# Kernel optimization log

Measured on AMD Instinct MI355X. Metric: run time of the kernel, lower is better.

## Reference

```python
import jax, jax.numpy as jnp
import numpy as np

B, L, H, V, HALF = 128, 4096, 64, 64, 32
ALPHA = 0.95
LN_EPS = 1e-5


def _normalize(x):
    # torch F.normalize(dim=-1): x / max(||x||_2, 1e-12)
    n = jnp.linalg.norm(x, axis=-1, keepdims=True)
    return x / jnp.maximum(n, 1e-12)


def setup_inputs() -> dict:
    key = jax.random.key(0)
    ks = jax.random.split(key, 17)
    s = 0.05
    return {
        "seq": jax.random.randint(ks[0], (B, L), 0, V),
        "embed": jax.random.normal(ks[1], (V, H), jnp.float32),
        "W1": jax.random.normal(ks[2], (H, 2 * H), jnp.float32) * s,
        "b1": jnp.zeros((2 * H,), jnp.float32),
        "W2": jax.random.normal(ks[3], (2 * H, H), jnp.float32) * s,
        "b2": jnp.zeros((H,), jnp.float32),
        "gamma": jnp.ones((H,), jnp.float32),
        "beta": jnp.zeros((H,), jnp.float32),
        "Ws": jax.random.normal(ks[4], (H, HALF), jnp.float32) * s,
        "bs": jnp.zeros((HALF,), jnp.float32),
        "We": jax.random.normal(ks[5], (H, HALF), jnp.float32) * s,
        "be": jnp.zeros((HALF,), jnp.float32),
        "Wrp": jax.random.normal(ks[6], (2 * HALF, H), jnp.float32) * s,
        "brp": jnp.zeros((H,), jnp.float32),
        "Wout": jax.random.normal(ks[7], (H, V), jnp.float32) * s,
        "bout": jnp.zeros((V,), jnp.float32),
    }


def _forward(seq, embed, W1, b1, W2, b2, gamma, beta,
             Ws, bs, We, be, Wrp, brp, Wout, bout):
    # Encoder: embed + FF(ReLU) residual + LayerNorm
    h0 = embed[seq]                                   # [B,L,H]
    ff = jnp.maximum(h0 @ W1 + b1, 0.0) @ W2 + b2
    x = h0 + ff
    mu = x.mean(-1, keepdims=True)
    var = ((x - mu) ** 2).mean(-1, keepdims=True)
    h = (x - mu) / jnp.sqrt(var + LN_EPS) * gamma + beta  # [B,L,H]

    # Precompute per-step projections for t = 0 .. L-2
    hp = h[:, :-1, :]                                 # [B,L-1,H]
    hs = hp @ Ws + bs                                 # [B,L-1,HALF]
    he = hp @ We + be
    ksn = _normalize(hs)
    ken = _normalize(he)
    scale = (jnp.arange(L - 1, dtype=h.dtype) + 1.0) / L  # (t+1)/L

    def step(carry, inp):
        M_s, M_e = carry                              # [B,HALF,HALF]
        hs_t, he_t, ks_t, ke_t, sc = inp
        vps = jnp.einsum('bij,bj->bi', M_s, ks_t)
        vpe = jnp.einsum('bij,bj->bi', M_e, ke_t)
        M_s = M_s + (1.0 - ALPHA) * (hs_t - vps)[:, :, None] * ks_t[:, None, :]
        M_e = M_e + (1.0 - ALPHA) * sc * (he_t - vpe)[:, :, None] * ke_t[:, None, :]
        return (M_s, M_e), None

    xs = (jnp.swapaxes(hs, 0, 1), jnp.swapaxes(he, 0, 1),
          jnp.swapaxes(ksn, 0, 1), jnp.swapaxes(ken, 0, 1), scale)
    M0 = jnp.zeros((B, HALF, HALF), h.dtype)
    (M_s, M_e), _ = jax.lax.scan(step, (M0, M0), xs)

    # Read with last-token query
    q = h[:, -1, :]
    qs = _normalize(q @ Ws + bs)
    qe = _normalize(q @ We + be)
    rs = jnp.einsum('bij,bj->bi', M_s, qs)
    re = jnp.einsum('bij,bj->bi', M_e, qe)
    r = jnp.concatenate([rs, re], axis=-1)            # [B,2*HALF]
    return (r @ Wrp + brp) @ Wout + bout              # [B,V]


def reference(seq, embed, W1, b1, W2, b2, gamma, beta,
              Ws, bs, We, be, Wrp, brp, Wout, bout):
    return _forward(seq, embed, W1, b1, W2, b2, gamma, beta,
                    Ws, bs, We, be, Wrp, brp, Wout, bout)
```

## Files before the change

### kernel.cpp

```cpp
#include <hip/hip_runtime.h>
#include <hip/hip_bf16.h>
#include <stdint.h>


#define BETA 0.05f
#define NB 128
#define NL 4096
#define TC 16
#define NCH 256
#define NBLD 6
#define SLOT_F 1360
#define NSLOT 12

#define L_GR   (NSLOT * SLOT_F)
#define L_DA   (L_GR + 4096)
#define L_RV   (L_DA + 64)
#define L_O1   (L_RV + 64)
#define L_WHO  (L_O1 + 64)
#define L_TOT  (L_WHO + 1)

struct Ptrs { const void* p[15]; };

__device__ inline float readlane_f(float v, int l) {
    return __int_as_float(__builtin_amdgcn_readlane(__float_as_int(v), l));
}
__device__ inline float bperm_f(int idx, float v) {
    return __int_as_float(__builtin_amdgcn_ds_bpermute(idx, __float_as_int(v)));
}
__device__ inline float ldT(const float* p, int i) { return p[i]; }
__device__ inline float ldT(const __hip_bfloat16* p, int i) { return __bfloat162float(p[i]); }

template <typename T>
__device__ void build_tables_body(const T* emb, const T* W1, const T* b1,
                                  const T* W2, const T* b2, const T* gam,
                                  const T* bet, const T* Wsm, const T* bsv,
                                  const T* Wem, const T* bev, float* tbl)
{
    int v = blockIdx.x;
    int j = threadIdx.x;
    __shared__ float h0s[64];
    __shared__ float act[128];
    __shared__ float hrow[64];

    float h0 = ldT(emb, v * 64 + j);
    h0s[j] = h0;
    __syncthreads();

    float za = ldT(b1, j);
    float zb = ldT(b1, j + 64);
    for (int k = 0; k < 64; ++k) {
        float hk = h0s[k];
        za = fmaf(hk, ldT(W1, k * 128 + j), za);
        zb = fmaf(hk, ldT(W1, k * 128 + j + 64), zb);
    }
    act[j] = fmaxf(za, 0.0f);
    act[j + 64] = fmaxf(zb, 0.0f);
    __syncthreads();

    float ff = ldT(b2, j);
    for (int k = 0; k < 128; ++k)
        ff = fmaf(act[k], ldT(W2, k * 64 + j), ff);
    float x = h0 + ff;

    float s = x;
    for (int off = 32; off >= 1; off >>= 1) s += __shfl_xor(s, off, 64);
    float mu = s * (1.0f / 64.0f);
    float d = x - mu;
    float s2 = d * d;
    for (int off = 32; off >= 1; off >>= 1) s2 += __shfl_xor(s2, off, 64);
    float var = s2 * (1.0f / 64.0f);
    float h = d / sqrtf(var + 1e-5f) * ldT(gam, j) + ldT(bet, j);
    hrow[j] = h;
    __syncthreads();

    if (j < 32) {
        float sv = ldT(bsv, j);
        for (int k = 0; k < 64; ++k)
            sv = fmaf(hrow[k], ldT(Wsm, k * 32 + j), sv);
        float n2 = sv * sv;
        for (int off = 16; off >= 1; off >>= 1) n2 += __shfl_xor(n2, off, 64);
        float nrm = fmaxf(sqrtf(n2), 1e-12f);
        tbl[v * 32 + j] = sv;
        tbl[2048 + v * 32 + j] = sv / nrm;
    } else {
        int jj = j - 32;
        float ev = ldT(bev, jj);
        for (int k = 0; k < 64; ++k)
            ev = fmaf(hrow[k], ldT(Wem, k * 32 + jj), ev);
        float n2 = ev * ev;
        for (int off = 16; off >= 1; off >>= 1) n2 += __shfl_xor(n2, off, 64);
        float nrm = fmaxf(sqrtf(n2), 1e-12f);
        tbl[4096 + v * 32 + jj] = ev;
        tbl[6144 + v * 32 + jj] = ev / nrm;
    }
}

__global__ __launch_bounds__(64, 2) void build_tables(Ptrs ps, float* __restrict__ tbl,
                                                      int* __restrict__ flags)
{
    if (blockIdx.x == 0) {
        flags[threadIdx.x] = 0;
        flags[threadIdx.x + 64] = 0;
    }
    uint32_t g0 = *(const uint32_t*)ps.p[5];
    if (g0 == 0x3F803F80u)
        build_tables_body((const __hip_bfloat16*)ps.p[0], (const __hip_bfloat16*)ps.p[1],
                          (const __hip_bfloat16*)ps.p[2], (const __hip_bfloat16*)ps.p[3],
                          (const __hip_bfloat16*)ps.p[4], (const __hip_bfloat16*)ps.p[5],
                          (const __hip_bfloat16*)ps.p[6], (const __hip_bfloat16*)ps.p[7],
                          (const __hip_bfloat16*)ps.p[8], (const __hip_bfloat16*)ps.p[9],
                          (const __hip_bfloat16*)ps.p[10], tbl);
    else
        build_tables_body((const float*)ps.p[0], (const float*)ps.p[1],
                          (const float*)ps.p[2], (const float*)ps.p[3],
                          (const float*)ps.p[4], (const float*)ps.p[5],
                          (const float*)ps.p[6], (const float*)ps.p[7],
                          (const float*)ps.p[8], (const float*)ps.p[9],
                          (const float*)ps.p[10], tbl);
}

__global__ __launch_bounds__(512, 1) void ema_ms(
    const int* __restrict__ seq, const float* __restrict__ tbl,
    Ptrs ps, float* __restrict__ rvbuf, int* __restrict__ flags,
    void* __restrict__ outv)
{
    __shared__ float S[L_TOT];

    int bm = blockIdx.x;
    int b = bm >> 1, mat = bm & 1;
    int tid = threadIdx.x;
    int wid = tid >> 6, lane = tid & 63;
    const float bstep = BETA / 4096.0f;

    if (tid < 64) S[L_DA + tid] = 0.0f;

    const float* ktab = tbl + 2048 + mat * 4096;
    for (int i = tid; i < 2048; i += 512)
        S[(i >> 5) * 33 + (i & 31)] = ktab[i];
    __syncthreads();

    {
        float Kown[32];
#pragma unroll
        for (int j = 0; j < 32; ++j) Kown[j] = S[lane * 33 + j];
        for (int v8 = 0; v8 < 8; ++v8) {
            int vt = wid * 8 + v8;
            float acc = 0.0f;
#pragma unroll
            for (int j = 0; j < 32; ++j)
                acc = fmaf(S[vt * 33 + j], Kown[j], acc);
            S[L_GR + vt * 64 + lane] = acc;
        }
    }
    __syncthreads();

    const int* sb = seq + (size_t)b * NL;
    float y = 0.0f;
    if (wid == 0) {
        int vlast = sb[NL - 1];
        y = S[L_GR + vlast * 64 + lane];
    }

    const int NRND = (NCH + NBLD - 1) / NBLD;

    for (int r = 0; r <= NRND; ++r) {
        if (wid != 0 && wid != 4) {
            int bi = (wid > 4) ? (wid - 2) : (wid - 1);
            int ci = NBLD * r + bi;
            if (r < NRND && ci < NCH) {
                int c = NCH - 1 - ci;
                float* slot = S + ((r & 1) * NBLD + bi) * SLOT_F;
                int tokv = 0; float bneg = 0.0f;
                if (lane < TC) {
                    int t = c * TC + (TC - 1) - lane;
                    tokv = sb[t];
                    float bb = mat ? bstep * (float)(t + 1) : BETA;
                    if (t == NL - 1) bb = 0.0f;
                    bneg = -bb;
                    ((int*)(slot + 1344))[lane] = tokv;
                }
                float garr[TC];
#pragma unroll
                for (int p = 0; p < TC; ++p) {
                    int vp = __builtin_amdgcn_readlane(tokv, p);
                    const float* gr = S + L_GR + vp * 64;
                    slot[320 + p * 64 + lane] = gr[lane];
                    garr[p] = gr[tokv] * bneg;
                }
                float x[TC];
                x[0] = (lane == 0) ? 1.0f : 0.0f;
#pragma unroll
                for (int p = 1; p < TC; ++p) {
                    float xp = (lane == p) ? 1.0f : 0.0f;
#pragma unroll
                    for (int j = 0; j < p; ++j)
                        xp = fmaf(readlane_f(garr[p], j), x[j], xp);
                    x[p] = xp;
                }
                if (lane < TC) {
#pragma unroll
                    for (int p = 0; p < TC; ++p)
                        slot[p * 20 + lane] = x[p];
                }
            }
        } else if (wid == 0 && r >= 1) {
            int rpar = ((r - 1) & 1) * NBLD;
            int base_ci = NBLD * (r - 1);
            int nch_r = NCH - base_ci;
            if (nch_r > NBLD) nch_r = NBLD;

            float* slot0 = S + rpar * SLOT_F;
            int tokc = ((int*)(slot0 + 1344))[lane & 15];
            const float4* vr0 = (const float4*)(slot0 + (lane & 15) * 20);
            float4 Vc0 = vr0[0], Vc1 = vr0[1], Vc2 = vr0[2], Vc3 = vr0[3];
            float gpc[16];
#pragma unroll
            for (int p = 0; p < 16; ++p)
                gpc[p] = slot0[320 + p * 64 + lane];

            for (int bi = 0; bi < nch_r; ++bi) {
                int c = NCH - 1 - (base_ci + bi);

                int bin = (bi + 1 < nch_r) ? (bi + 1) : bi;
                float* slotn = S + (rpar + bin) * SLOT_F;
                int tokn = ((int*)(slotn + 1344))[lane & 15];
                const float4* vrn = (const float4*)(slotn + (lane & 15) * 20);
                float4 Vn0 = vrn[0], Vn1 = vrn[1], Vn2 = vrn[2], Vn3 = vrn[3];
                float gpn[16];
#pragma unroll
                for (int p = 0; p < 16; ++p)
                    gpn[p] = slotn[320 + p * 64 + lane];
                asm volatile("" ::: "memory");

                float ry = bperm_f(tokc << 2, y);
                float bv = 0.0f;
                if (lane < TC) {
                    int t = c * TC + (TC - 1) - lane;
                    float bb = mat ? bstep * (float)(t + 1) : BETA;
                    if (t == NL - 1) bb = 0.0f;
                    bv = bb;
                }
                float s0 = Vc0.x * readlane_f(ry, 0);
                float s1 = Vc0.y * readlane_f(ry, 1);
                float s2 = Vc0.z * readlane_f(ry, 2);
                float s3 = Vc0.w * readlane_f(ry, 3);
                s0 = fmaf(Vc1.x, readlane_f(ry, 4), s0);
                s1 = fmaf(Vc1.y, readlane_f(ry, 5), s1);
                s2 = fmaf(Vc1.z, readlane_f(ry, 6), s2);
                s3 = fmaf(Vc1.w, readlane_f(ry, 7), s3);
                s0 = fmaf(Vc2.x, readlane_f(ry, 8), s0);
                s1 = fmaf(Vc2.y, readlane_f(ry, 9), s1);
                s2 = fmaf(Vc2.z, readlane_f(ry, 10), s2);
                s3 = fmaf(Vc2.w, readlane_f(ry, 11), s3);
                s0 = fmaf(Vc3.x, readlane_f(ry, 12), s0);
                s1 = fmaf(Vc3.y, readlane_f(ry, 13), s1);
                s2 = fmaf(Vc3.z, readlane_f(ry, 14), s2);
                s3 = fmaf(Vc3.w, readlane_f(ry, 15), s3);
                float dv = ((s0 + s1) + (s2 + s3)) * bv;
                float dn = -dv;
                float ya = 0.f, yb = 0.f, yc2 = 0.f, yd = 0.f;
#pragma unroll
                for (int p = 0; p < TC; p += 4) {
                    ya  = fmaf(readlane_f(dn, p),     gpc[p],     ya);
                    yb  = fmaf(readlane_f(dn, p + 1), gpc[p + 1], yb);
                    yc2 = fmaf(readlane_f(dn, p + 2), gpc[p + 2], yc2);
                    yd  = fmaf(readlane_f(dn, p + 3), gpc[p + 3], yd);
                }
                y += (ya + yb) + (yc2 + yd);
                if (lane < TC) atomicAdd(&S[L_DA + tokc], dv);

                tokc = tokn;
                Vc0 = Vn0; Vc1 = Vn1; Vc2 = Vn2; Vc3 = Vn3;
#pragma unroll
                for (int p = 0; p < 16; ++p) gpc[p] = gpn[p];
            }
        }
        __syncthreads();
    }

    if (tid < 32) {
        float rr = 0.0f;
        const float* hsrc = tbl + mat * 4096;
        for (int v = 0; v < 64; ++v)
            rr = fmaf(S[L_DA + v], hsrc[v * 32 + tid], rr);
        __hip_atomic_store(&rvbuf[bm * 32 + tid], rr,
                           __ATOMIC_RELAXED, __HIP_MEMORY_SCOPE_AGENT);
    }
    __syncthreads();
    if (tid == 0) {
        int old = __hip_atomic_fetch_add(&flags[b], 1,
                                         __ATOMIC_ACQ_REL, __HIP_MEMORY_SCOPE_AGENT);
        ((int*)S)[L_WHO] = old;
    }
    __syncthreads();
    if (((int*)S)[L_WHO] != 1) return;

    if (tid < 64)
        S[L_RV + tid] = __hip_atomic_load(&rvbuf[b * 64 + tid],
                                          __ATOMIC_RELAXED, __HIP_MEMORY_SCOPE_AGENT);
    __syncthreads();

    uint32_t g0h = *(const uint32_t*)ps.p[5];
    int isbf = (g0h == 0x3F803F80u) ? 1 : 0;
    if (tid < 64) {
        float o;
        if (isbf) {
            const __hip_bfloat16* W = (const __hip_bfloat16*)ps.p[11];
            o = __bfloat162float(((const __hip_bfloat16*)ps.p[12])[tid]);
            for (int i = 0; i < 64; ++i)
                o = fmaf(S[L_RV + i], __bfloat162float(W[i * 64 + tid]), o);
        } else {
            const float* W = (const float*)ps.p[11];
            o = ((const float*)ps.p[12])[tid];
            for (int i = 0; i < 64; ++i)
                o = fmaf(S[L_RV + i], W[i * 64 + tid], o);
        }
        S[L_O1 + tid] = o;
    }
    __syncthreads();
    if (tid < 64) {
        float o2;
        if (isbf) {
            const __hip_bfloat16* W = (const __hip_bfloat16*)ps.p[13];
            o2 = __bfloat162float(((const __hip_bfloat16*)ps.p[14])[tid]);
            for (int i = 0; i < 64; ++i)
                o2 = fmaf(S[L_O1 + i], __bfloat162float(W[i * 64 + tid]), o2);
            ((__hip_bfloat16*)outv)[b * 64 + tid] = __float2bfloat16(o2);
        } else {
            const float* W = (const float*)ps.p[13];
            o2 = ((const float*)ps.p[14])[tid];
            for (int i = 0; i < 64; ++i)
                o2 = fmaf(S[L_O1 + i], W[i * 64 + tid], o2);
            ((float*)outv)[b * 64 + tid] = o2;
        }
    }
}

extern "C" void kernel_launch(void* const* d_in, const int* in_sizes, int n_in,
                              void* d_out, int out_size, void* d_ws, size_t ws_size,
                              hipStream_t stream) {
    const int* seq = (const int*)d_in[0];
    Ptrs ps;
    for (int i = 0; i < 15; ++i) ps.p[i] = d_in[i + 1];

    float* tbl = (float*)d_ws;
    float* rvbuf = tbl + 8192;
    int* flags = (int*)(rvbuf + 8192);

    build_tables<<<64, 64, 0, stream>>>(ps, tbl, flags);
    ema_ms<<<NB * 2, 512, 0, stream>>>(seq, tbl, ps, rvbuf, flags, d_out);
}
```

Measured before the change: 195.6 us.

## Use all non-master waves as chunk builders and replace bpermute with scalar readlanes

Raises the number of builder waves per round from six to seven, so the previously idle wave 4 now also builds chunk solutions, and grows the LDS slot count to match. In the serial consumer wave, the per-chunk ds_bpermute gather of y by token is replaced with readlanes indexed by scalar token ids, which are extracted ahead of time from the prefetched next slot. The aim is fewer rounds and less latency on the sequential critical path, at the cost of more LDS and more scalar registers for the token arrays.

```diff
diff --git a/kernel.cpp b/kernel.cpp
--- a/kernel.cpp
+++ b/kernel.cpp
@@ -8,9 +8,9 @@
 #define NL 4096
 #define TC 16
 #define NCH 256
-#define NBLD 6
+#define NBLD 7
 #define SLOT_F 1360
-#define NSLOT 12
+#define NSLOT 14
 
 #define L_GR   (NSLOT * SLOT_F)
 #define L_DA   (L_GR + 4096)
@@ -23,9 +23,6 @@
 
 __device__ inline float readlane_f(float v, int l) {
     return __int_as_float(__builtin_amdgcn_readlane(__float_as_int(v), l));
-}
-__device__ inline float bperm_f(int idx, float v) {
-    return __int_as_float(__builtin_amdgcn_ds_bpermute(idx, __float_as_int(v)));
 }
 __device__ inline float ldT(const float* p, int i) { return p[i]; }
 __device__ inline float ldT(const __hip_bfloat16* p, int i) { return __bfloat162float(p[i]); }
@@ -164,8 +161,8 @@
     const int NRND = (NCH + NBLD - 1) / NBLD;
 
     for (int r = 0; r <= NRND; ++r) {
-        if (wid != 0 && wid != 4) {
-            int bi = (wid > 4) ? (wid - 2) : (wid - 1);
+        if (wid != 0) {
+            int bi = wid - 1;
             int ci = NBLD * r + bi;
             if (r < NRND && ci < NCH) {
                 int c = NCH - 1 - ci;
@@ -203,7 +200,7 @@
                         slot[p * 20 + lane] = x[p];
                 }
             }
-        } else if (wid == 0 && r >= 1) {
+        } else if (r >= 1) {
             int rpar = ((r - 1) & 1) * NBLD;
             int base_ci = NBLD * (r - 1);
             int nch_r = NCH - base_ci;
@@ -211,6 +208,10 @@
 
             float* slot0 = S + rpar * SLOT_F;
             int tokc = ((int*)(slot0 + 1344))[lane & 15];
+            int stokc[16];
+#pragma unroll
+            for (int q = 0; q < 16; ++q)
+                stokc[q] = __builtin_amdgcn_readlane(tokc, q);
             const float4* vr0 = (const float4*)(slot0 + (lane & 15) * 20);
             float4 Vc0 = vr0[0], Vc1 = vr0[1], Vc2 = vr0[2], Vc3 = vr0[3];
             float gpc[16];
@@ -224,6 +225,10 @@
                 int bin = (bi + 1 < nch_r) ? (bi + 1) : bi;
                 float* slotn = S + (rpar + bin) * SLOT_F;
                 int tokn = ((int*)(slotn + 1344))[lane & 15];
+                int stokn[16];
+#pragma unroll
+                for (int q = 0; q < 16; ++q)
+                    stokn[q] = __builtin_amdgcn_readlane(tokn, q);
                 const float4* vrn = (const float4*)(slotn + (lane & 15) * 20);
                 float4 Vn0 = vrn[0], Vn1 = vrn[1], Vn2 = vrn[2], Vn3 = vrn[3];
                 float gpn[16];
@@ -232,7 +237,6 @@
                     gpn[p] = slotn[320 + p * 64 + lane];
                 asm volatile("" ::: "memory");
 
-                float ry = bperm_f(tokc << 2, y);
                 float bv = 0.0f;
                 if (lane < TC) {
                     int t = c * TC + (TC - 1) - lane;
@@ -240,22 +244,26 @@
                     if (t == NL - 1) bb = 0.0f;
                     bv = bb;
                 }
-                float s0 = Vc0.x * readlane_f(ry, 0);
-                float s1 = Vc0.y * readlane_f(ry, 1);
-                float s2 = Vc0.z * readlane_f(ry, 2);
-                float s3 = Vc0.w * readlane_f(ry, 3);
-                s0 = fmaf(Vc1.x, readlane_f(ry, 4), s0);
-                s1 = fmaf(Vc1.y, readlane_f(ry, 5), s1);
-                s2 = fmaf(Vc1.z, readlane_f(ry, 6), s2);
-                s3 = fmaf(Vc1.w, readlane_f(ry, 7), s3);
-                s0 = fmaf(Vc2.x, readlane_f(ry, 8), s0);
-                s1 = fmaf(Vc2.y, readlane_f(ry, 9), s1);
-                s2 = fmaf(Vc2.z, readlane_f(ry, 10), s2);
-                s3 = fmaf(Vc2.w, readlane_f(ry, 11), s3);
-                s0 = fmaf(Vc3.x, readlane_f(ry, 12), s0);
-                s1 = fmaf(Vc3.y, readlane_f(ry, 13), s1);
-                s2 = fmaf(Vc3.z, readlane_f(ry, 14), s2);
-                s3 = fmaf(Vc3.w, readlane_f(ry, 15), s3);
+                float ryq[16];
+#pragma unroll
+                for (int q = 0; q < 16; ++q)
+                    ryq[q] = readlane_f(y, stokc[q]);
+                float s0 = Vc0.x * ryq[0];
+                float s1 = Vc0.y * ryq[1];
+                float s2 = Vc0.z * ryq[2];
+                float s3 = Vc0.w * ryq[3];
+                s0 = fmaf(Vc1.x, ryq[4], s0);
+                s1 = fmaf(Vc1.y, ryq[5], s1);
+                s2 = fmaf(Vc1.z, ryq[6], s2);
+                s3 = fmaf(Vc1.w, ryq[7], s3);
+                s0 = fmaf(Vc2.x, ryq[8], s0);
+                s1 = fmaf(Vc2.y, ryq[9], s1);
+                s2 = fmaf(Vc2.z, ryq[10], s2);
+                s3 = fmaf(Vc2.w, ryq[11], s3);
+                s0 = fmaf(Vc3.x, ryq[12], s0);
+                s1 = fmaf(Vc3.y, ryq[13], s1);
+                s2 = fmaf(Vc3.z, ryq[14], s2);
+                s3 = fmaf(Vc3.w, ryq[15], s3);
                 float dv = ((s0 + s1) + (s2 + s3)) * bv;
                 float dn = -dv;
                 float ya = 0.f, yb = 0.f, yc2 = 0.f, yd = 0.f;
@@ -270,6 +278,8 @@
                 if (lane < TC) atomicAdd(&S[L_DA + tokc], dv);
 
                 tokc = tokn;
+#pragma unroll
+                for (int q = 0; q < 16; ++q) stokc[q] = stokn[q];
                 Vc0 = Vn0; Vc1 = Vn1; Vc2 = Vn2; Vc3 = Vn3;
 #pragma unroll
                 for (int p = 0; p < 16; ++p) gpc[p] = gpn[p];
```

Measured after the change: 213.6 us. 9.3% more time.
